# Performance work log

Measured on AMD Instinct MI355X. Metric: run time of the kernel, lower is better.

Reference implementation:

```python
import jax, jax.numpy as jnp
import numpy as np

CHUNK = 1024  # chunk over N to avoid materializing the full [B,N,M] distance matrix


def _min_dists(xyz1, xyz2):
    """For each point in xyz1 [B,N,3], squared L2 distance to nearest point in xyz2 [B,M,3].
    Returns [B,N]. Computed in chunks of N to bound peak memory."""
    B, N, _ = xyz1.shape
    y2 = jnp.sum(xyz2 * xyz2, axis=-1)  # [B,M]
    n_chunks = N // CHUNK
    # [n_chunks, B, CHUNK, 3]
    xc = jnp.transpose(xyz1.reshape(B, n_chunks, CHUNK, 3), (1, 0, 2, 3))

    def chunk_min(x):  # x: [B,CHUNK,3]
        x2 = jnp.sum(x * x, axis=-1)  # [B,CHUNK]
        xy = jnp.einsum('bcd,bmd->bcm', x, xyz2)  # [B,CHUNK,M]
        d = x2[:, :, None] + y2[:, None, :] - 2.0 * xy
        return jnp.min(d, axis=-1)  # [B,CHUNK]

    mins = jax.lax.map(chunk_min, xc)  # [n_chunks, B, CHUNK]
    return jnp.transpose(mins, (1, 0, 2)).reshape(B, N)


def setup_inputs() -> dict:
    key = jax.random.key(0)
    k1, k2 = jax.random.split(key)
    xyz1 = jax.random.normal(k1, (8, 8192, 3), dtype=jnp.float32)
    xyz2 = jax.random.normal(k2, (8, 8192, 3), dtype=jnp.float32)
    return {"xyz1": xyz1, "xyz2": xyz2}


def reference(xyz1, xyz2):
    # ChamferDistanceL2.forward with ignore_zeros=False and batch>1:
    # only dist1 (xyz1 -> nearest in xyz2) is used; return its mean.
    dist1 = _min_dists(xyz1, xyz2)  # [B,N]
    return jnp.mean(dist1)
```

## Files before the change

kernel.cpp:

```cpp
#include <hip/hip_runtime.h>

typedef _Float16 v8h __attribute__((ext_vector_type(8)));
typedef float v16f __attribute__((ext_vector_type(16)));

#define BB 8
#define NN 8192
#define MM 8192
#define SPLITM 8
#define CPTS 1024
#define JTC 32
#define TPB 256
#define NI 2


__device__ __forceinline__ float min3f(float a, float b, float c) {
    return fminf(fminf(a, b), c);
}

__global__ __launch_bounds__(TPB, 4) void chamfer_min_mfma(const float* __restrict__ xyz1,
                                                           const float* __restrict__ xyz2,
                                                           float* __restrict__ pmins) {
    __shared__ v8h aLds[CPTS];

    int ig     = blockIdx.x & 31;
    int jchunk = (blockIdx.x >> 5) & 7;
    int b      = blockIdx.x >> 8;
    int t = threadIdx.x;
    int wid = t >> 6;
    int lane = t & 63;
    int laneq = lane & 31;
    int half = lane >> 5;

    const float* srcA = xyz2 + ((size_t)b * MM + (size_t)jchunk * CPTS) * 3;
#pragma unroll
    for (int k = 0; k < CPTS / TPB; ++k) {
        int p = k * TPB + t;
        float x = srcA[p * 3 + 0], y = srcA[p * 3 + 1], z = srcA[p * 3 + 2];
        _Float16 h0 = (_Float16)x, h1 = (_Float16)y, h2 = (_Float16)z;
        float y0 = (float)h0, y1 = (float)h1, y2v = (float)h2;
        float s = fmaf(y0, y0, fmaf(y1, y1, y2v * y2v));
        _Float16 shi = (_Float16)s;
        _Float16 slo = (_Float16)(s - (float)shi);
        v8h v = {h0, h1, h2, shi, slo, (_Float16)1.0f, (_Float16)1.0f, (_Float16)0.0f};
        aLds[p] = v;
    }

    int it0 = (ig * 4 + wid) * NI;
    v8h bf[NI];
#pragma unroll
    for (int tt = 0; tt < NI; ++tt) {
        int i = (it0 + tt) * 32 + laneq;
        const float* p = xyz1 + ((size_t)b * NN + i) * 3;
        _Float16 h0 = (_Float16)p[0], h1 = (_Float16)p[1], h2 = (_Float16)p[2];
        float x0 = (float)h0, x1 = (float)h1, x2v = (float)h2;
        float s = fmaf(x0, x0, fmaf(x1, x1, x2v * x2v));
        _Float16 shi = (_Float16)s;
        _Float16 slo = (_Float16)(s - (float)shi);
        v8h v = {};
        if (half == 0) {
            v[0] = (_Float16)(-2.0f * x0);
            v[1] = (_Float16)(-2.0f * x1);
            v[2] = (_Float16)(-2.0f * x2v);
            v[3] = (_Float16)1.0f; v[4] = (_Float16)1.0f;
            v[5] = shi; v[6] = slo;
        }
        bf[tt] = v;
    }

    __syncthreads();

    const v16f zc = {};
    float mg[NI][4];
#pragma unroll
    for (int tt = 0; tt < NI; ++tt)
#pragma unroll
        for (int g = 0; g < 4; ++g) mg[tt][g] = 1e30f;

    int jt0 = wid * 8;
    v8h a_next = aLds[jt0 * 32 + laneq];
#pragma unroll 1
    for (int s = 0; s < JTC; ++s) {
        v8h a = a_next;
        int jn = ((s + 1) & (JTC - 1)) * 32;
        int jtn = (jn + jt0 * 32) & (CPTS - 1);
        a_next = aLds[jtn + laneq];
        v16f c[NI];
#pragma unroll
        for (int tt = 0; tt < NI; ++tt)
            c[tt] = __builtin_amdgcn_mfma_f32_32x32x16_f16(a, bf[tt], zc, 0, 0, 0);
#pragma unroll
        for (int tt = 0; tt < NI; ++tt)
#pragma unroll
            for (int g = 0; g < 4; ++g) {
                int r = 4 * g;
                mg[tt][g] = min3f(min3f(c[tt][r], c[tt][r + 1], c[tt][r + 2]),
                                  c[tt][r + 3], mg[tt][g]);
            }
    }

    float m0 = fminf(min3f(mg[0][0], mg[0][1], mg[0][2]), mg[0][3]);
    float m1 = fminf(min3f(mg[1][0], mg[1][1], mg[1][2]), mg[1][3]);
    m0 = fminf(m0, __shfl_xor(m0, 32));
    m1 = fminf(m1, __shfl_xor(m1, 32));
    int i = (it0 + half) * 32 + laneq;
    pmins[(size_t)jchunk * (BB * NN) + (size_t)b * NN + i] = half ? m1 : m0;
}

__global__ __launch_bounds__(256) void chamfer_reduce(const float* __restrict__ pmins,
                                                      float* __restrict__ out) {
    int i = blockIdx.x * 256 + threadIdx.x;
    float m = pmins[i];
#pragma unroll
    for (int sp = 1; sp < SPLITM; ++sp)
        m = fminf(m, pmins[(size_t)sp * (BB * NN) + i]);
    float s = m;
#pragma unroll
    for (int off = 32; off > 0; off >>= 1) s += __shfl_down(s, off);
    __shared__ float ls[4];
    int lane = threadIdx.x & 63, wv = threadIdx.x >> 6;
    if (lane == 0) ls[wv] = s;
    __syncthreads();
    if (threadIdx.x == 0) {
        float tt = (ls[0] + ls[1]) + (ls[2] + ls[3]);
        atomicAdd(out, tt * (1.0f / (float)(BB * NN)));
    }
}

extern "C" void kernel_launch(void* const* d_in, const int* in_sizes, int n_in,
                              void* d_out, int out_size, void* d_ws, size_t ws_size,
                              hipStream_t stream) {
    const float* xyz1 = (const float*)d_in[0];
    const float* xyz2 = (const float*)d_in[1];
    float* out = (float*)d_out;
    float* pmins = (float*)d_ws;

    hipMemsetAsync(out, 0, sizeof(float), stream);
    chamfer_min_mfma<<<BB * SPLITM * 32, TPB, 0, stream>>>(xyz1, xyz2, pmins);
    chamfer_reduce<<<(BB * NN) / 256, 256, 0, stream>>>(pmins, out);
}
```

Before: 76.87 us.

## Fuse min and mean into one kernel iterating all of xyz2 with double-buffered LDS

Each block now owns 128 query points and loops over all eight 1024-point chunks of xyz2 itself, instead of splitting M across blocks. Chunk loads are double-buffered: the next chunk is read into registers while MFMAs run on the current LDS buffer. This removes the partial-min workspace and the second reduce kernel, and the block's sum goes straight to the atomic. In exchange the grid shrinks from 2048 to 512 blocks, there is one MFMA per step instead of two, and a barrier is added per chunk, which may cut parallelism and latency hiding.

After: 85.33 us. +11.0%, slower.

```diff
diff --git a/kernel.cpp b/kernel.cpp
--- a/kernel.cpp
+++ b/kernel.cpp
@@ -6,124 +6,117 @@
 #define BB 8
 #define NN 8192
 #define MM 8192
-#define SPLITM 8
 #define CPTS 1024
-#define JTC 32
+#define NCH (MM / CPTS)
 #define TPB 256
-#define NI 2
+#define GRID (BB * (NN / 128))
 
 
 __device__ __forceinline__ float min3f(float a, float b, float c) {
     return fminf(fminf(a, b), c);
 }
 
-__global__ __launch_bounds__(TPB, 4) void chamfer_min_mfma(const float* __restrict__ xyz1,
-                                                           const float* __restrict__ xyz2,
-                                                           float* __restrict__ pmins) {
-    __shared__ v8h aLds[CPTS];
+__device__ __forceinline__ v8h packA(float x, float y, float z) {
+    _Float16 h0 = (_Float16)x, h1 = (_Float16)y, h2 = (_Float16)z;
+    float y0 = (float)h0, y1 = (float)h1, y2v = (float)h2;
+    float s = fmaf(y0, y0, fmaf(y1, y1, y2v * y2v));
+    _Float16 shi = (_Float16)s;
+    _Float16 slo = (_Float16)(s - (float)shi);
+    v8h v = {h0, h1, h2, shi, slo, (_Float16)1.0f, (_Float16)1.0f, (_Float16)0.0f};
+    return v;
+}
 
-    int ig     = blockIdx.x & 31;
-    int jchunk = (blockIdx.x >> 5) & 7;
-    int b      = blockIdx.x >> 8;
-    int t = threadIdx.x;
-    int wid = t >> 6;
-    int lane = t & 63;
+__global__ __launch_bounds__(TPB, 2) void chamfer_fused(const float* __restrict__ xyz1,
+                                                        const float* __restrict__ xyz2,
+                                                        float* __restrict__ out) {
+    __shared__ v8h aB[2][CPTS];
+    __shared__ float ls[4];
+
+    int g     = blockIdx.x & 63;
+    int b     = blockIdx.x >> 6;
+    int t     = threadIdx.x;
+    int wid   = t >> 6;
+    int lane  = t & 63;
     int laneq = lane & 31;
-    int half = lane >> 5;
+    int half  = lane >> 5;
 
-    const float* srcA = xyz2 + ((size_t)b * MM + (size_t)jchunk * CPTS) * 3;
-#pragma unroll
-    for (int k = 0; k < CPTS / TPB; ++k) {
-        int p = k * TPB + t;
-        float x = srcA[p * 3 + 0], y = srcA[p * 3 + 1], z = srcA[p * 3 + 2];
-        _Float16 h0 = (_Float16)x, h1 = (_Float16)y, h2 = (_Float16)z;
-        float y0 = (float)h0, y1 = (float)h1, y2v = (float)h2;
-        float s = fmaf(y0, y0, fmaf(y1, y1, y2v * y2v));
-        _Float16 shi = (_Float16)s;
-        _Float16 slo = (_Float16)(s - (float)shi);
-        v8h v = {h0, h1, h2, shi, slo, (_Float16)1.0f, (_Float16)1.0f, (_Float16)0.0f};
-        aLds[p] = v;
-    }
-
-    int it0 = (ig * 4 + wid) * NI;
-    v8h bf[NI];
-#pragma unroll
-    for (int tt = 0; tt < NI; ++tt) {
-        int i = (it0 + tt) * 32 + laneq;
+    v8h bf = {};
+    int i = (g * 4 + wid) * 32 + laneq;
+    {
         const float* p = xyz1 + ((size_t)b * NN + i) * 3;
         _Float16 h0 = (_Float16)p[0], h1 = (_Float16)p[1], h2 = (_Float16)p[2];
         float x0 = (float)h0, x1 = (float)h1, x2v = (float)h2;
         float s = fmaf(x0, x0, fmaf(x1, x1, x2v * x2v));
         _Float16 shi = (_Float16)s;
         _Float16 slo = (_Float16)(s - (float)shi);
-        v8h v = {};
         if (half == 0) {
-            v[0] = (_Float16)(-2.0f * x0);
-            v[1] = (_Float16)(-2.0f * x1);
-            v[2] = (_Float16)(-2.0f * x2v);
-            v[3] = (_Float16)1.0f; v[4] = (_Float16)1.0f;
-            v[5] = shi; v[6] = slo;
+            bf[0] = (_Float16)(-2.0f * x0);
+            bf[1] = (_Float16)(-2.0f * x1);
+            bf[2] = (_Float16)(-2.0f * x2v);
+            bf[3] = (_Float16)1.0f;
+            bf[4] = (_Float16)1.0f;
+            bf[5] = shi;
+            bf[6] = slo;
         }
-        bf[tt] = v;
     }
 
+    const float* srcB = xyz2 + (size_t)b * (MM * 3);
+
+#pragma unroll
+    for (int k = 0; k < CPTS / TPB; ++k) {
+        int p = k * TPB + t;
+        aB[0][p] = packA(srcB[p * 3 + 0], srcB[p * 3 + 1], srcB[p * 3 + 2]);
+    }
     __syncthreads();
 
     const v16f zc = {};
-    float mg[NI][4];
+    float mg[4] = {1e30f, 1e30f, 1e30f, 1e30f};
+    int rot = wid * 8;
+
+#pragma unroll 2
+    for (int c = 0; c < NCH; ++c) {
+        float r[12];
+        if (c + 1 < NCH) {
+            const float* sN = srcB + (size_t)(c + 1) * (CPTS * 3);
 #pragma unroll
-    for (int tt = 0; tt < NI; ++tt)
+            for (int k = 0; k < 4; ++k) {
+                int p = k * TPB + t;
+                r[3 * k + 0] = sN[p * 3 + 0];
+                r[3 * k + 1] = sN[p * 3 + 1];
+                r[3 * k + 2] = sN[p * 3 + 2];
+            }
+        }
+
+        const v8h* A = aB[c & 1];
+#pragma unroll 8
+        for (int s = 0; s < 32; ++s) {
+            v8h a = A[(((s + rot) & 31) << 5) + laneq];
+            v16f d = __builtin_amdgcn_mfma_f32_32x32x16_f16(a, bf, zc, 0, 0, 0);
 #pragma unroll
-        for (int g = 0; g < 4; ++g) mg[tt][g] = 1e30f;
+            for (int q = 0; q < 4; ++q) {
+                int rr = 4 * q;
+                mg[q] = min3f(min3f(d[rr], d[rr + 1], d[rr + 2]), d[rr + 3], mg[q]);
+            }
+        }
 
-    int jt0 = wid * 8;
-    v8h a_next = aLds[jt0 * 32 + laneq];
-#pragma unroll 1
-    for (int s = 0; s < JTC; ++s) {
-        v8h a = a_next;
-        int jn = ((s + 1) & (JTC - 1)) * 32;
-        int jtn = (jn + jt0 * 32) & (CPTS - 1);
-        a_next = aLds[jtn + laneq];
-        v16f c[NI];
+        if (c + 1 < NCH) {
+            v8h* W = aB[(c + 1) & 1];
 #pragma unroll
-        for (int tt = 0; tt < NI; ++tt)
-            c[tt] = __builtin_amdgcn_mfma_f32_32x32x16_f16(a, bf[tt], zc, 0, 0, 0);
-#pragma unroll
-        for (int tt = 0; tt < NI; ++tt)
-#pragma unroll
-            for (int g = 0; g < 4; ++g) {
-                int r = 4 * g;
-                mg[tt][g] = min3f(min3f(c[tt][r], c[tt][r + 1], c[tt][r + 2]),
-                                  c[tt][r + 3], mg[tt][g]);
-            }
+            for (int k = 0; k < 4; ++k)
+                W[k * TPB + t] = packA(r[3 * k + 0], r[3 * k + 1], r[3 * k + 2]);
+        }
+        __syncthreads();
     }
 
-    float m0 = fminf(min3f(mg[0][0], mg[0][1], mg[0][2]), mg[0][3]);
-    float m1 = fminf(min3f(mg[1][0], mg[1][1], mg[1][2]), mg[1][3]);
+    float m0 = fminf(min3f(mg[0], mg[1], mg[2]), mg[3]);
     m0 = fminf(m0, __shfl_xor(m0, 32));
-    m1 = fminf(m1, __shfl_xor(m1, 32));
-    int i = (it0 + half) * 32 + laneq;
-    pmins[(size_t)jchunk * (BB * NN) + (size_t)b * NN + i] = half ? m1 : m0;
-}
-
-__global__ __launch_bounds__(256) void chamfer_reduce(const float* __restrict__ pmins,
-                                                      float* __restrict__ out) {
-    int i = blockIdx.x * 256 + threadIdx.x;
-    float m = pmins[i];
+    float sum = half ? 0.0f : m0;
 #pragma unroll
-    for (int sp = 1; sp < SPLITM; ++sp)
-        m = fminf(m, pmins[(size_t)sp * (BB * NN) + i]);
-    float s = m;
-#pragma unroll
-    for (int off = 32; off > 0; off >>= 1) s += __shfl_down(s, off);
-    __shared__ float ls[4];
-    int lane = threadIdx.x & 63, wv = threadIdx.x >> 6;
-    if (lane == 0) ls[wv] = s;
+    for (int off = 32; off > 0; off >>= 1) sum += __shfl_xor(sum, off);
+    if (lane == 0) ls[wid] = sum;
     __syncthreads();
-    if (threadIdx.x == 0) {
-        float tt = (ls[0] + ls[1]) + (ls[2] + ls[3]);
-        atomicAdd(out, tt * (1.0f / (float)(BB * NN)));
-    }
+    if (t == 0)
+        atomicAdd(out, ((ls[0] + ls[1]) + (ls[2] + ls[3])) * (1.0f / (float)(BB * NN)));
 }
 
 extern "C" void kernel_launch(void* const* d_in, const int* in_sizes, int n_in,
@@ -132,9 +125,8 @@
     const float* xyz1 = (const float*)d_in[0];
     const float* xyz2 = (const float*)d_in[1];
     float* out = (float*)d_out;
-    float* pmins = (float*)d_ws;
-
+    (void)d_ws;
+    (void)ws_size;
     hipMemsetAsync(out, 0, sizeof(float), stream);
-    chamfer_min_mfma<<<BB * SPLITM * 32, TPB, 0, stream>>>(xyz1, xyz2, pmins);
-    chamfer_reduce<<<(BB * NN) / 256, 256, 0, stream>>>(pmins, out);
+    chamfer_fused<<<GRID, TPB, 0, stream>>>(xyz1, xyz2, out);
 }
```
